# Optimization experiments

Measured on AMD Instinct MI355X. Metric: run time of the kernel, lower is better.

## Reference

```python
import jax, jax.numpy as jnp
import numpy as np

NUM_HEADS = 8
LN_EPS = 1e-5


def setup_inputs() -> dict:
    key = jax.random.key(0)
    ks = jax.random.split(key, 5)
    B, C, H, W = 4, 256, 48, 48
    scale = 1.0 / np.sqrt(C)
    return {
        "x": jax.random.normal(ks[0], (B, C, H, W), dtype=jnp.float32),
        "Wq": jax.random.normal(ks[1], (C, C), dtype=jnp.float32) * scale,
        "Wk": jax.random.normal(ks[2], (C, C), dtype=jnp.float32) * scale,
        "Wv": jax.random.normal(ks[3], (C, C), dtype=jnp.float32) * scale,
        "Wo": jax.random.normal(ks[4], (C, C), dtype=jnp.float32) * scale,
        "gamma": jnp.ones((C,), dtype=jnp.float32),
        "beta": jnp.zeros((C,), dtype=jnp.float32),
    }


def reference(x, Wq, Wk, Wv, Wo, gamma, beta):
    B, C, H, W = x.shape
    hd = C // NUM_HEADS
    N = H * W
    xf = x.reshape(B, C, N)  # [B, C, N]
    # 1x1 conv (no bias) == channel matmul, then split heads: [B, h, d, N]
    def proj(Wm):
        return jnp.einsum('oc,bcn->bon', Wm, xf).reshape(B, NUM_HEADS, hd, N)
    q = proj(Wq)
    k = proj(Wk)
    v = proj(Wv)
    # scores[b,h,i,j] = sum_d q[b,h,d,i] k[b,h,d,j] / sqrt(hd)
    scores = jnp.einsum('bhdi,bhdj->bhij', q, k) / jnp.sqrt(jnp.float32(hd))
    attn = jax.nn.softmax(scores, axis=-1)  # [B, h, N, N]
    # attended[b,h,d,i] = sum_j v[b,h,d,j] attn[b,h,i,j]
    attended = jnp.einsum('bhdj,bhij->bhdi', v, attn).reshape(B, C, H, W)
    out = jnp.einsum('oc,bchw->bohw', Wo, attended) + x
    # LayerNorm over channels (applied in NHWC layout in original)
    mu = out.mean(axis=1, keepdims=True)
    var = out.var(axis=1, keepdims=True)
    out = (out - mu) * jax.lax.rsqrt(var + LN_EPS)
    out = out * gamma[None, :, None, None] + beta[None, :, None, None]
    return out
```

## Files before the change

### kernel.cpp

```cpp
#include <hip/hip_runtime.h>

#define DEVI __device__ __forceinline__

typedef __bf16 bf16x8 __attribute__((ext_vector_type(8)));
typedef float f32x4 __attribute__((ext_vector_type(4)));

#define QSCALE 0.25503488f

#if __has_builtin(__builtin_amdgcn_exp2f)
#define EXP2(x) __builtin_amdgcn_exp2f(x)
#else
#define EXP2(x) __expf(0.69314718055994531f * (x))
#endif

DEVI unsigned short bfbits(float f) {
  union { __bf16 h; unsigned short u; } x;
  x.h = (__bf16)f;
  return x.u;
}
DEVI unsigned packbf2(float a, float b) {
  return (unsigned)bfbits(a) | ((unsigned)bfbits(b) << 16);
}
DEVI float bflo(unsigned u) { return __uint_as_float(u << 16); }
DEVI float bfhi(unsigned u) { return __uint_as_float(u & 0xffff0000u); }

DEVI void gload16(const unsigned short* g, void* l) {
  __builtin_amdgcn_global_load_lds((__attribute__((address_space(1))) const unsigned*)g,
                                   (__attribute__((address_space(3))) unsigned*)l, 16, 0, 0);
}

__global__ __launch_bounds__(256) void k_prep_x(const float* __restrict__ x,
                                                unsigned short* __restrict__ xT) {
  __shared__ float tile[64][65];
  const int b = blockIdx.x, n0 = blockIdx.y * 64, c0 = blockIdx.z * 64;
  const int t = threadIdx.x, tn = t & 63, tg = t >> 6;
  const float* xp = x + ((size_t)b * 256 + c0) * 2304 + n0;
#pragma unroll
  for (int i = 0; i < 16; ++i) {
    const int c = tg * 16 + i;
    tile[c][tn] = xp[(size_t)c * 2304 + tn];
  }
  __syncthreads();
  unsigned short* op = xT + ((size_t)b * 2304 + n0) * 256 + c0;
#pragma unroll
  for (int i = 0; i < 16; ++i) {
    const int n = tg * 16 + i;
    op[(size_t)n * 256 + tn] = bfbits(tile[tn][n]);
  }
}

__global__ __launch_bounds__(256) void k_prep_wo(const float* __restrict__ Wo,
                                                 unsigned short* __restrict__ WoB) {
  const int i = (blockIdx.x * 256 + threadIdx.x) * 4;
  const float4 v = *(const float4*)(Wo + i);
  uint2 u;
  u.x = packbf2(v.x, v.y);
  u.y = packbf2(v.z, v.w);
  *(uint2*)(WoB + i) = u;
}

__global__ __launch_bounds__(256) void k_proj_qk(const unsigned short* __restrict__ xT,
                                                 const float* __restrict__ Wq,
                                                 const float* __restrict__ Wk,
                                                 unsigned short* __restrict__ qhm,
                                                 unsigned short* __restrict__ khm) {
  __shared__ __align__(16) unsigned char wlds[32768];
  const int l = threadIdx.x & 63, w = threadIdx.x >> 6;
  const int lr = l & 15, lg = l >> 4;
  const int row0 = blockIdx.x * 64 + w * 16;
  const int h = blockIdx.y;
  {
    const int t = threadIdx.x;
    const int mat = t >> 7;
    const int t2 = t & 127;
    const int row = t2 >> 2;
    const int cj0 = (t2 & 3) * 8;
    const float* wp = (mat ? Wk : Wq) + (size_t)(h * 32 + row) * 256;
    unsigned char* ldst = wlds + mat * 16384 + row * 512;
#pragma unroll
    for (int i = 0; i < 8; ++i) {
      const int cj = cj0 + i;
      const float4 v0 = *(const float4*)(wp + cj * 8);
      const float4 v1 = *(const float4*)(wp + cj * 8 + 4);
      uint4 u;
      u.x = packbf2(v0.x, v0.y);
      u.y = packbf2(v0.z, v0.w);
      u.z = packbf2(v1.x, v1.y);
      u.w = packbf2(v1.z, v1.w);
      *(uint4*)(ldst + ((cj * 16) ^ ((row & 7) << 4))) = u;
    }
  }
  __syncthreads();

  f32x4 acc[2][2];
#pragma unroll
  for (int i = 0; i < 2; ++i)
#pragma unroll
    for (int j = 0; j < 2; ++j) acc[i][j] = (f32x4){0.f, 0.f, 0.f, 0.f};
  for (int ks = 0; ks < 8; ++ks) {
    const int c = ks * 32 + lg * 8;
    const bf16x8 a = *(const bf16x8*)(xT + (size_t)(row0 + lr) * 256 + c);
    bf16x8 bfr[2][2];
#pragma unroll
    for (int ot = 0; ot < 2; ++ot) {
      const int brow = ot * 16 + lr;
      const unsigned off = (unsigned)(brow * 512) + (((unsigned)((ks * 4 + lg) * 16)) ^ ((brow & 7) << 4));
      bfr[0][ot] = *(const bf16x8*)(wlds + off);
      bfr[1][ot] = *(const bf16x8*)(wlds + 16384 + off);
    }
#pragma unroll
    for (int m = 0; m < 2; ++m)
#pragma unroll
      for (int ot = 0; ot < 2; ++ot)
        acc[m][ot] = __builtin_amdgcn_mfma_f32_16x16x32_bf16(a, bfr[m][ot], acc[m][ot], 0, 0, 0);
  }
  const int b = row0 / 2304;
  const int nloc = row0 - b * 2304;
  const size_t slab = (size_t)(b * 8 + h) * 2304;
#pragma unroll
  for (int m = 0; m < 2; ++m) {
    unsigned short* outp = m ? khm : qhm;
    const float scale = m ? 1.0f : QSCALE;
#pragma unroll
    for (int ot = 0; ot < 2; ++ot)
#pragma unroll
      for (int r = 0; r < 4; ++r) {
        const int n = nloc + lg * 4 + r;
        const int d = ot * 16 + lr;
        outp[(slab + n) * 32 + d] = bfbits(acc[m][ot][r] * scale);
      }
  }
}

__global__ __launch_bounds__(256) void k_proj_v(const unsigned short* __restrict__ xT,
                                                const float* __restrict__ Wv,
                                                unsigned short* __restrict__ vN) {
  __shared__ __align__(16) unsigned char wlds[32768];
  const int l = threadIdx.x & 63, w = threadIdx.x >> 6;
  const int lr = l & 15, lg = l >> 4;
  const int rowbase = blockIdx.x * 64;
  const int col0 = blockIdx.y * 32;
  {
    const int t = threadIdx.x;
    const int row = t >> 2;
    const int cj0 = (t & 3) * 8;
    const float* wp = Wv + (size_t)(rowbase + row) * 256;
    unsigned char* ldst = wlds + row * 512;
#pragma unroll
    for (int i = 0; i < 8; ++i) {
      const int cj = cj0 + i;
      const float4 v0 = *(const float4*)(wp + cj * 8);
      const float4 v1 = *(const float4*)(wp + cj * 8 + 4);
      uint4 u;
      u.x = packbf2(v0.x, v0.y);
      u.y = packbf2(v0.z, v0.w);
      u.z = packbf2(v1.x, v1.y);
      u.w = packbf2(v1.z, v1.w);
      *(uint4*)(ldst + ((cj * 16) ^ ((row & 7) << 4))) = u;
    }
  }
  __syncthreads();

  f32x4 acc[2];
  acc[0] = (f32x4){0.f, 0.f, 0.f, 0.f};
  acc[1] = (f32x4){0.f, 0.f, 0.f, 0.f};
  for (int ks = 0; ks < 8; ++ks) {
    const int c = ks * 32 + lg * 8;
    bf16x8 a, bfr[2];
    const int arow = w * 16 + lr;
    a = *(const bf16x8*)(wlds + arow * 512 + (((unsigned)((ks * 4 + lg) * 16)) ^ ((arow & 7) << 4)));
#pragma unroll
    for (int nt = 0; nt < 2; ++nt)
      bfr[nt] = *(const bf16x8*)(xT + (size_t)(col0 + nt * 16 + lr) * 256 + c);
#pragma unroll
    for (int nt = 0; nt < 2; ++nt)
      acc[nt] = __builtin_amdgcn_mfma_f32_16x16x32_bf16(a, bfr[nt], acc[nt], 0, 0, 0);
  }
  const int b = blockIdx.y / 72, nb = (blockIdx.y % 72) * 32;
#pragma unroll
  for (int nt = 0; nt < 2; ++nt)
#pragma unroll
    for (int r = 0; r < 4; ++r) {
      const int o = rowbase + w * 16 + lg * 4 + r;
      const int n = nb + nt * 16 + lr;
      vN[(size_t)b * 589824 + (size_t)o * 2304 + n] = bfbits(acc[nt][r]);
    }
}

template <bool DIRECT>
__global__ __launch_bounds__(256) void k_attn(const unsigned short* __restrict__ qhm,
                                              const unsigned short* __restrict__ khm,
                                              const unsigned short* __restrict__ vN,
                                              unsigned short* __restrict__ partO,
                                              float* __restrict__ partS,
                                              unsigned short* __restrict__ attT,
                                              int tpc) {
  __shared__ __align__(16) unsigned char sm[32768];
  const int l = threadIdx.x & 63, w = threadIdx.x >> 6;
  const int lr = l & 15, lg = l >> 4;
  const int bh = blockIdx.y, b = bh >> 3, h = bh & 7;
  const int i0 = blockIdx.x * 128 + w * 32;
  const int c = blockIdx.z, t0 = c * tpc;
  unsigned char* smw = sm + w * 4096;
  const size_t slab = (size_t)bh * 2304;

  bf16x8 qf[2];
  {
    const unsigned short* qbase = qhm + (slab + i0) * 32;
#pragma unroll
    for (int it = 0; it < 2; ++it)
      qf[it] = *(const bf16x8*)(qbase + (it * 16 + lr) * 32 + lg * 8);
  }

  bf16x8 ones;
#pragma unroll
  for (int e = 0; e < 8; ++e) ones[e] = (__bf16)1.0f;

  f32x4 oacc[2][2];
#pragma unroll
  for (int i = 0; i < 2; ++i)
#pragma unroll
    for (int j = 0; j < 2; ++j) oacc[i][j] = (f32x4){0.f, 0.f, 0.f, 0.f};
  f32x4 psum[2];
  psum[0] = (f32x4){0.f, 0.f, 0.f, 0.f};
  psum[1] = (f32x4){0.f, 0.f, 0.f, 0.f};

  const unsigned short* kbase = khm + slab * 32 + (size_t)(64 * w + (l ^ ((l >> 2) & 3))) * 8;
  const int vks = w >> 1;
  const int vlg = (w * 2 + (l >> 5)) & 3;
  const unsigned short* vsrc = vN + (size_t)(b * 256 + h * 32 + (l & 31)) * 2304 + vks * 32 + vlg * 8;
  const int kdst = 16384 + w * 1024;
  const int vdst = 24576 + w * 1024;
  const int kxor = ((lg ^ (lr & 3)) << 4);

  gload16(kbase + (size_t)t0 * 2048, sm + kdst);
  gload16(vsrc + t0 * 64, sm + vdst);
  __syncthreads();

  for (int tt = 0; tt < tpc; ++tt) {
    const int buf = tt & 1;
    if (tt < tpc - 1) {
      const int nbuf = (tt + 1) & 1;
      gload16(kbase + (size_t)(t0 + tt + 1) * 2048, sm + kdst + nbuf * 4096);
      gload16(vsrc + (t0 + tt + 1) * 64, sm + vdst + nbuf * 4096);
    }

    const unsigned char* kb = sm + 16384 + buf * 4096;
    const unsigned char* vb = sm + 24576 + buf * 4096;

    bf16x8 kf[4];
    {
      const unsigned char* kread = kb + lr * 64 + kxor;
#pragma unroll
      for (int jt = 0; jt < 4; ++jt)
        kf[jt] = *(const bf16x8*)(kread + jt * 1024);
    }

    f32x4 s[4][2];
    const f32x4 zf = (f32x4){0.f, 0.f, 0.f, 0.f};
#pragma unroll
    for (int jt = 0; jt < 4; ++jt)
#pragma unroll
      for (int it = 0; it < 2; ++it)
        s[jt][it] = __builtin_amdgcn_mfma_f32_16x16x32_bf16(kf[jt], qf[it], zf, 0, 0, 0);

#pragma unroll
    for (int it = 0; it < 2; ++it) {
      const int iloc = it * 16 + lr;
      const unsigned swz = (unsigned)((iloc & 7) << 4);
      unsigned char* prow = smw + iloc * 128;
#pragma unroll
      for (int jt = 0; jt < 4; ++jt) {
        const float p0 = EXP2(s[jt][it][0]);
        const float p1 = EXP2(s[jt][it][1]);
        const float p2 = EXP2(s[jt][it][2]);
        const float p3 = EXP2(s[jt][it][3]);
        const unsigned jb = (unsigned)(jt * 32 + lg * 8);
        uint2 u;
        u.x = packbf2(p0, p1);
        u.y = packbf2(p2, p3);
        *(uint2*)(prow + (jb ^ swz)) = u;
      }
    }

    bf16x8 vf[2][2], pf[2][2];
#pragma unroll
    for (int dt = 0; dt < 2; ++dt)
#pragma unroll
      for (int ks = 0; ks < 2; ++ks)
        vf[dt][ks] = *(const bf16x8*)(vb + ks * 2048 + lg * 512 + (dt * 16 + lr) * 16);
#pragma unroll
    for (int it = 0; it < 2; ++it) {
      const int iloc = it * 16 + lr;
      const unsigned swz = (unsigned)((iloc & 7) << 4);
#pragma unroll
      for (int ks = 0; ks < 2; ++ks)
        pf[it][ks] = *(const bf16x8*)(smw + iloc * 128 + ((unsigned)(ks * 64 + lg * 16) ^ swz));
    }
#pragma unroll
    for (int dt = 0; dt < 2; ++dt)
#pragma unroll
      for (int it = 0; it < 2; ++it) {
        oacc[dt][it] = __builtin_amdgcn_mfma_f32_16x16x32_bf16(vf[dt][0], pf[it][0], oacc[dt][it], 0, 0, 0);
        oacc[dt][it] = __builtin_amdgcn_mfma_f32_16x16x32_bf16(vf[dt][1], pf[it][1], oacc[dt][it], 0, 0, 0);
      }
#pragma unroll
    for (int it = 0; it < 2; ++it) {
      psum[it] = __builtin_amdgcn_mfma_f32_16x16x32_bf16(ones, pf[it][0], psum[it], 0, 0, 0);
      psum[it] = __builtin_amdgcn_mfma_f32_16x16x32_bf16(ones, pf[it][1], psum[it], 0, 0, 0);
    }
    __syncthreads();
  }

  if (DIRECT) {
#pragma unroll
    for (int it = 0; it < 2; ++it) {
      const float inv = 1.0f / psum[it][0];
      const int iloc = it * 16 + lr;
      unsigned char* orow = smw + iloc * 68;
#pragma unroll
      for (int dt = 0; dt < 2; ++dt) {
        const int d = dt * 16 + lg * 4;
        *(unsigned*)(orow + d * 2) = packbf2(oacc[dt][it][0] * inv, oacc[dt][it][1] * inv);
        *(unsigned*)(orow + d * 2 + 4) = packbf2(oacc[dt][it][2] * inv, oacc[dt][it][3] * inv);
      }
    }
    __syncthreads();
    unsigned* attu = (unsigned*)attT;
#pragma unroll
    for (int it2 = 0; it2 < 8; ++it2) {
      const int lin = it2 * 64 + l;
      const int row = lin >> 4, k = lin & 15;
      const unsigned u = *(const unsigned*)(smw + row * 68 + k * 4);
      attu[(size_t)(b * 2304 + i0 + row) * 128 + h * 16 + k] = u;
    }
  } else {
    const size_t pbase = ((size_t)(c * 32 + bh) * 2304 + i0) * 32;
#pragma unroll
    for (int it = 0; it < 2; ++it)
#pragma unroll
      for (int dt = 0; dt < 2; ++dt) {
        const size_t addr = pbase + (size_t)(it * 16 + lr) * 32 + dt * 16 + lg * 4;
        uint2 u;
        u.x = packbf2(oacc[dt][it][0], oacc[dt][it][1]);
        u.y = packbf2(oacc[dt][it][2], oacc[dt][it][3]);
        *(uint2*)(partO + addr) = u;
      }
    if (lg == 0) {
      const size_t sbase = (size_t)(c * 32 + bh) * 2304 + i0;
      partS[sbase + lr] = psum[0][0];
      partS[sbase + 16 + lr] = psum[1][0];
    }
  }
}

template <bool COMBINE>
__global__ __launch_bounds__(256) void k_out_ln(const unsigned short* __restrict__ Wo,
                                                const unsigned short* __restrict__ attT,
                                                const unsigned short* __restrict__ partO,
                                                const float* __restrict__ partS,
                                                int nc,
                                                const float* __restrict__ x,
                                                const float* __restrict__ gamma,
                                                const float* __restrict__ beta,
                                                float* __restrict__ out) {
  __shared__ __align__(16) unsigned char alds[8192];
  __shared__ float wsum[4][16], wsq[4][16], smean[16], srstd[16];
  const int l = threadIdx.x & 63, w = threadIdx.x >> 6;
  const int lr = l & 15, lg = l >> 4;
  const int b = blockIdx.x / 144;
  const int n0 = (blockIdx.x % 144) * 16;
  const int row0 = w * 64;
  const size_t bn0 = (size_t)b * 2304 + n0;

  if (COMBINE) {
    const int t = threadIdx.x;
    const int row = t >> 4;
    const int i = n0 + row;
    const int cj0 = (t & 15) * 2;
#pragma unroll
    for (int ii = 0; ii < 2; ++ii) {
      const int cj = cj0 + ii;
      const int h = cj >> 2;
      const int d0 = (cj & 3) * 8;
      const int bh8 = b * 8 + h;
      float ssum = 0.f;
      float a0 = 0.f, a1 = 0.f, a2 = 0.f, a3 = 0.f, a4 = 0.f, a5 = 0.f, a6 = 0.f, a7 = 0.f;
      for (int cz = 0; cz < nc; ++cz) {
        const size_t rbase = (size_t)(cz * 32 + bh8) * 2304 + i;
        ssum += partS[rbase];
        const uint4 v = *(const uint4*)(partO + rbase * 32 + d0);
        a0 += bflo(v.x); a1 += bfhi(v.x);
        a2 += bflo(v.y); a3 += bfhi(v.y);
        a4 += bflo(v.z); a5 += bfhi(v.z);
        a6 += bflo(v.w); a7 += bfhi(v.w);
      }
      const float inv = 1.0f / ssum;
      uint4 u;
      u.x = packbf2(a0 * inv, a1 * inv);
      u.y = packbf2(a2 * inv, a3 * inv);
      u.z = packbf2(a4 * inv, a5 * inv);
      u.w = packbf2(a6 * inv, a7 * inv);
      *(uint4*)(alds + row * 512 + ((cj * 16) ^ ((row & 7) << 4))) = u;
    }
  } else {
    const int t = threadIdx.x;
    const int row = t >> 4;
    const int cj0 = (t & 15) * 2;
#pragma unroll
    for (int ii = 0; ii < 2; ++ii) {
      const int cj = cj0 + ii;
      const uint4 v = *(const uint4*)(attT + (bn0 + row) * 256 + cj * 8);
      *(uint4*)(alds + row * 512 + ((cj * 16) ^ ((row & 7) << 4))) = v;
    }
  }
  __syncthreads();

  f32x4 acc[4];
#pragma unroll
  for (int i = 0; i < 4; ++i) acc[i] = (f32x4){0.f, 0.f, 0.f, 0.f};
  for (int ks = 0; ks < 8; ++ks) {
    const int c = ks * 32 + lg * 8;
    bf16x8 a[4], bb;
#pragma unroll
    for (int rt = 0; rt < 4; ++rt)
      a[rt] = *(const bf16x8*)(Wo + (size_t)(row0 + rt * 16 + lr) * 256 + c);
    bb = *(const bf16x8*)(alds + lr * 512 + (((unsigned)((ks * 4 + lg) * 16)) ^ ((lr & 7) << 4)));
#pragma unroll
    for (int rt = 0; rt < 4; ++rt)
      acc[rt] = __builtin_amdgcn_mfma_f32_16x16x32_bf16(a[rt], bb, acc[rt], 0, 0, 0);
  }
  const float* xb = x + (size_t)b * 589824;
  float vals[4][4];
  float s0 = 0.f, q0 = 0.f;
#pragma unroll
  for (int rt = 0; rt < 4; ++rt)
#pragma unroll
    for (int r = 0; r < 4; ++r) {
      const int o = row0 + rt * 16 + lg * 4 + r;
      const int n = n0 + lr;
      const float vv = acc[rt][r] + xb[(size_t)o * 2304 + n];
      vals[rt][r] = vv;
      s0 += vv;
      q0 += vv * vv;
    }
  s0 += __shfl_xor(s0, 16); s0 += __shfl_xor(s0, 32);
  q0 += __shfl_xor(q0, 16); q0 += __shfl_xor(q0, 32);
  if (l < 16) {
    wsum[w][l] = s0;
    wsq[w][l] = q0;
  }
  __syncthreads();
  if (threadIdx.x < 16) {
    const int c16 = threadIdx.x;
    const float S = wsum[0][c16] + wsum[1][c16] + wsum[2][c16] + wsum[3][c16];
    const float Q = wsq[0][c16] + wsq[1][c16] + wsq[2][c16] + wsq[3][c16];
    const float mean = S * (1.0f / 256.0f);
    const float var = Q * (1.0f / 256.0f) - mean * mean;
    smean[c16] = mean;
    srstd[c16] = rsqrtf(var + 1e-5f);
  }
  __syncthreads();
  {
    const float mean = smean[lr];
    const float rstd = srstd[lr];
    const int n = n0 + lr;
#pragma unroll
    for (int rt = 0; rt < 4; ++rt)
#pragma unroll
      for (int r = 0; r < 4; ++r) {
        const int o = row0 + rt * 16 + lg * 4 + r;
        out[(size_t)b * 589824 + (size_t)o * 2304 + n] =
            (vals[rt][r] - mean) * rstd * gamma[o] + beta[o];
      }
  }
}

extern "C" void kernel_launch(void* const* d_in, const int* in_sizes, int n_in,
                              void* d_out, int out_size, void* d_ws, size_t ws_size,
                              hipStream_t stream) {
  (void)in_sizes; (void)n_in; (void)out_size;
  const float* x = (const float*)d_in[0];
  const float* Wq = (const float*)d_in[1];
  const float* Wk = (const float*)d_in[2];
  const float* Wv = (const float*)d_in[3];
  const float* Wo = (const float*)d_in[4];
  const float* gamma = (const float*)d_in[5];
  const float* beta = (const float*)d_in[6];
  float* out = (float*)d_out;
  char* ws = (char*)d_ws;
  unsigned short* attT = (unsigned short*)(ws);
  unsigned short* qhm = (unsigned short*)(ws + 4718592);
  unsigned short* khm = (unsigned short*)(ws + 9437184);
  unsigned short* vN = (unsigned short*)(ws + 14155776);
  unsigned short* xT = (unsigned short*)(ws + 18874368);
  unsigned short* WoB = qhm;

  const size_t base = 18874368;
  const size_t chunk = 4718592 + 294912;
  const size_t need4 = base + 4 * chunk;
  const size_t need2 = base + 2 * chunk;
  const int nc = (ws_size >= need4) ? 4 : (ws_size >= need2) ? 2 : 1;
  unsigned short* partO = (unsigned short*)(ws + base);
  float* partS = (float*)(ws + base + (size_t)nc * 4718592);

  k_prep_x<<<dim3(4, 36, 4), 256, 0, stream>>>(x, xT);
  k_proj_qk<<<dim3(144, 8), 256, 0, stream>>>(xT, Wq, Wk, qhm, khm);
  k_proj_v<<<dim3(4, 288), 256, 0, stream>>>(xT, Wv, vN);
  if (nc > 1) {
    k_attn<false><<<dim3(18, 32, nc), 256, 0, stream>>>(qhm, khm, vN, partO, partS, attT, 36 / nc);
    k_prep_wo<<<dim3(64), 256, 0, stream>>>(Wo, WoB);
    k_out_ln<true><<<dim3(576), 256, 0, stream>>>(WoB, attT, partO, partS, nc, x, gamma, beta, out);
  } else {
    k_attn<true><<<dim3(18, 32, 1), 256, 0, stream>>>(qhm, khm, vN, attT, (float*)attT, attT, 36);
    k_prep_wo<<<dim3(64), 256, 0, stream>>>(Wo, WoB);
    k_out_ln<false><<<dim3(576), 256, 0, stream>>>(WoB, attT, partO, partS, 1, x, gamma, beta, out);
  }
}
```

Baseline: 171.3 us.

## Fuse x transpose, QKV projections and Wo conversion into one kernel

Replaces the separate x-transpose, Q/K projection, V projection and Wo-conversion kernels with a single kernel. Each of the 144 blocks transposes a 64-position tile of x into a bf16 LDS tile and computes Q, K and V for all heads from it, so the xT workspace round trip and three launches go away. 16 extra blocks convert Wo. The cost is a grid of only 160 blocks of 256 threads with about 96KB of LDS each, which lowers parallelism and occupancy, and each block now serialises loops over all weight chunks.

```diff
diff --git a/kernel.cpp b/kernel.cpp
--- a/kernel.cpp
+++ b/kernel.cpp
@@ -29,162 +29,167 @@
                                    (__attribute__((address_space(3))) unsigned*)l, 16, 0, 0);
 }
 
-__global__ __launch_bounds__(256) void k_prep_x(const float* __restrict__ x,
-                                                unsigned short* __restrict__ xT) {
-  __shared__ float tile[64][65];
-  const int b = blockIdx.x, n0 = blockIdx.y * 64, c0 = blockIdx.z * 64;
-  const int t = threadIdx.x, tn = t & 63, tg = t >> 6;
-  const float* xp = x + ((size_t)b * 256 + c0) * 2304 + n0;
-#pragma unroll
-  for (int i = 0; i < 16; ++i) {
-    const int c = tg * 16 + i;
-    tile[c][tn] = xp[(size_t)c * 2304 + tn];
-  }
-  __syncthreads();
-  unsigned short* op = xT + ((size_t)b * 2304 + n0) * 256 + c0;
-#pragma unroll
-  for (int i = 0; i < 16; ++i) {
-    const int n = tg * 16 + i;
-    op[(size_t)n * 256 + tn] = bfbits(tile[tn][n]);
-  }
-}
-
-__global__ __launch_bounds__(256) void k_prep_wo(const float* __restrict__ Wo,
-                                                 unsigned short* __restrict__ WoB) {
-  const int i = (blockIdx.x * 256 + threadIdx.x) * 4;
-  const float4 v = *(const float4*)(Wo + i);
-  uint2 u;
-  u.x = packbf2(v.x, v.y);
-  u.y = packbf2(v.z, v.w);
-  *(uint2*)(WoB + i) = u;
-}
-
-__global__ __launch_bounds__(256) void k_proj_qk(const unsigned short* __restrict__ xT,
-                                                 const float* __restrict__ Wq,
-                                                 const float* __restrict__ Wk,
-                                                 unsigned short* __restrict__ qhm,
-                                                 unsigned short* __restrict__ khm) {
-  __shared__ __align__(16) unsigned char wlds[32768];
-  const int l = threadIdx.x & 63, w = threadIdx.x >> 6;
+__global__ __launch_bounds__(256) void k_qkv(const float* __restrict__ x,
+                                             const float* __restrict__ Wq,
+                                             const float* __restrict__ Wk,
+                                             const float* __restrict__ Wv,
+                                             const float* __restrict__ Wo,
+                                             unsigned short* __restrict__ qhm,
+                                             unsigned short* __restrict__ khm,
+                                             unsigned short* __restrict__ vN,
+                                             unsigned short* __restrict__ WoB) {
+  const int bid = blockIdx.x;
+  const int t = threadIdx.x;
+  if (bid >= 144) {
+    const int i = ((bid - 144) * 256 + t) * 16;
+#pragma unroll
+    for (int j = 0; j < 4; ++j) {
+      const float4 v = *(const float4*)(Wo + i + j * 4);
+      uint2 u;
+      u.x = packbf2(v.x, v.y);
+      u.y = packbf2(v.z, v.w);
+      *(uint2*)(WoB + i + j * 4) = u;
+    }
+    return;
+  }
+  __shared__ __align__(16) unsigned char xtile[32768];
+  __shared__ __align__(16) unsigned char wtile[32768];
+  __shared__ __align__(16) unsigned char wtile2[32768];
+  const int b = bid / 36, n0 = (bid % 36) * 64;
+  const int l = t & 63, w = t >> 6;
   const int lr = l & 15, lg = l >> 4;
-  const int row0 = blockIdx.x * 64 + w * 16;
-  const int h = blockIdx.y;
-  {
-    const int t = threadIdx.x;
-    const int mat = t >> 7;
-    const int t2 = t & 127;
-    const int row = t2 >> 2;
-    const int cj0 = (t2 & 3) * 8;
-    const float* wp = (mat ? Wk : Wq) + (size_t)(h * 32 + row) * 256;
-    unsigned char* ldst = wlds + mat * 16384 + row * 512;
-#pragma unroll
-    for (int i = 0; i < 8; ++i) {
-      const int cj = cj0 + i;
-      const float4 v0 = *(const float4*)(wp + cj * 8);
-      const float4 v1 = *(const float4*)(wp + cj * 8 + 4);
-      uint4 u;
-      u.x = packbf2(v0.x, v0.y);
-      u.y = packbf2(v0.z, v0.w);
-      u.z = packbf2(v1.x, v1.y);
-      u.w = packbf2(v1.z, v1.w);
-      *(uint4*)(ldst + ((cj * 16) ^ ((row & 7) << 4))) = u;
-    }
-  }
-  __syncthreads();
-
-  f32x4 acc[2][2];
-#pragma unroll
-  for (int i = 0; i < 2; ++i)
-#pragma unroll
-    for (int j = 0; j < 2; ++j) acc[i][j] = (f32x4){0.f, 0.f, 0.f, 0.f};
-  for (int ks = 0; ks < 8; ++ks) {
-    const int c = ks * 32 + lg * 8;
-    const bf16x8 a = *(const bf16x8*)(xT + (size_t)(row0 + lr) * 256 + c);
-    bf16x8 bfr[2][2];
-#pragma unroll
-    for (int ot = 0; ot < 2; ++ot) {
-      const int brow = ot * 16 + lr;
-      const unsigned off = (unsigned)(brow * 512) + (((unsigned)((ks * 4 + lg) * 16)) ^ ((brow & 7) << 4));
-      bfr[0][ot] = *(const bf16x8*)(wlds + off);
-      bfr[1][ot] = *(const bf16x8*)(wlds + 16384 + off);
-    }
-#pragma unroll
-    for (int m = 0; m < 2; ++m)
-#pragma unroll
-      for (int ot = 0; ot < 2; ++ot)
-        acc[m][ot] = __builtin_amdgcn_mfma_f32_16x16x32_bf16(a, bfr[m][ot], acc[m][ot], 0, 0, 0);
-  }
-  const int b = row0 / 2304;
-  const int nloc = row0 - b * 2304;
-  const size_t slab = (size_t)(b * 8 + h) * 2304;
-#pragma unroll
-  for (int m = 0; m < 2; ++m) {
-    unsigned short* outp = m ? khm : qhm;
-    const float scale = m ? 1.0f : QSCALE;
-#pragma unroll
-    for (int ot = 0; ot < 2; ++ot)
+  const int tn = t & 63, tg = t >> 6;
+
+  float* tmp = (float*)wtile;
+  for (int cb = 0; cb < 4; ++cb) {
+    const float* xp = x + ((size_t)b * 256 + cb * 64) * 2304 + n0;
+#pragma unroll
+    for (int i = 0; i < 16; ++i) {
+      const int c = tg * 16 + i;
+      tmp[c * 65 + tn] = xp[(size_t)c * 2304 + tn];
+    }
+    __syncthreads();
+    {
+      unsigned u[8];
+#pragma unroll
+      for (int j = 0; j < 8; ++j)
+        u[j] = packbf2(tmp[(tg * 16 + 2 * j) * 65 + tn], tmp[(tg * 16 + 2 * j + 1) * 65 + tn]);
+      unsigned char* dst = xtile + tn * 512;
+      const unsigned base = (unsigned)(cb * 128 + tg * 32);
+      const unsigned swz = (unsigned)((tn & 7) << 4);
+      *(uint4*)(dst + (base ^ swz)) = *(uint4*)&u[0];
+      *(uint4*)(dst + ((base + 16) ^ swz)) = *(uint4*)&u[4];
+    }
+    __syncthreads();
+  }
+
+  bf16x8 a[8];
+#pragma unroll
+  for (int ks = 0; ks < 8; ++ks)
+    a[ks] = *(const bf16x8*)(xtile + (w * 16 + lr) * 512 +
+                             (((unsigned)((ks * 4 + lg) * 16)) ^ ((lr & 7) << 4)));
+
+  for (int oc = 0; oc < 4; ++oc) {
+    {
+      const int mat = t >> 7;
+      const int t2 = t & 127;
+      const int row = t2 >> 1;
+      const int cj0 = (t2 & 1) * 16;
+      const float* wp = (mat ? Wk : Wq) + (size_t)(oc * 64 + row) * 256;
+      unsigned char* ldst = (mat ? wtile2 : wtile) + row * 512;
+      const unsigned swz = (unsigned)((row & 7) << 4);
+#pragma unroll
+      for (int i = 0; i < 16; ++i) {
+        const int cj = cj0 + i;
+        const float4 v0 = *(const float4*)(wp + cj * 8);
+        const float4 v1 = *(const float4*)(wp + cj * 8 + 4);
+        uint4 u;
+        u.x = packbf2(v0.x, v0.y);
+        u.y = packbf2(v0.z, v0.w);
+        u.z = packbf2(v1.x, v1.y);
+        u.w = packbf2(v1.z, v1.w);
+        *(uint4*)(ldst + (((unsigned)(cj * 16)) ^ swz)) = u;
+      }
+    }
+    __syncthreads();
+#pragma unroll
+    for (int m = 0; m < 2; ++m) {
+      const unsigned char* wsrc = m ? wtile2 : wtile;
+      unsigned short* outp = m ? khm : qhm;
+      const float scale = m ? 1.0f : QSCALE;
+      f32x4 acc[4];
+#pragma unroll
+      for (int ot = 0; ot < 4; ++ot) acc[ot] = (f32x4){0.f, 0.f, 0.f, 0.f};
+      for (int ks = 0; ks < 8; ++ks) {
+#pragma unroll
+        for (int ot = 0; ot < 4; ++ot) {
+          const int brow = ot * 16 + lr;
+          const bf16x8 bfr = *(const bf16x8*)(wsrc + brow * 512 +
+                                              (((unsigned)((ks * 4 + lg) * 16)) ^ ((brow & 7) << 4)));
+          acc[ot] = __builtin_amdgcn_mfma_f32_16x16x32_bf16(a[ks], bfr, acc[ot], 0, 0, 0);
+        }
+      }
+#pragma unroll
+      for (int ot = 0; ot < 4; ++ot) {
+        const int h = 2 * oc + (ot >> 1);
+        const int d = (ot & 1) * 16 + lr;
+        const size_t slab = (size_t)(b * 8 + h) * 2304;
+#pragma unroll
+        for (int r = 0; r < 4; ++r) {
+          const int n = n0 + w * 16 + lg * 4 + r;
+          outp[(slab + n) * 32 + d] = bfbits(acc[ot][r] * scale);
+        }
+      }
+    }
+    __syncthreads();
+  }
+
+  for (int oc = 0; oc < 4; ++oc) {
+    {
+      const int row = t >> 2;
+      const int cj0 = (t & 3) * 8;
+      const float* wp = Wv + (size_t)(oc * 64 + row) * 256;
+      unsigned char* ldst = wtile + row * 512;
+      const unsigned swz = (unsigned)((row & 7) << 4);
+#pragma unroll
+      for (int i = 0; i < 8; ++i) {
+        const int cj = cj0 + i;
+        const float4 v0 = *(const float4*)(wp + cj * 8);
+        const float4 v1 = *(const float4*)(wp + cj * 8 + 4);
+        uint4 u;
+        u.x = packbf2(v0.x, v0.y);
+        u.y = packbf2(v0.z, v0.w);
+        u.z = packbf2(v1.x, v1.y);
+        u.w = packbf2(v1.z, v1.w);
+        *(uint4*)(ldst + (((unsigned)(cj * 16)) ^ swz)) = u;
+      }
+    }
+    __syncthreads();
+    f32x4 acc[4];
+#pragma unroll
+    for (int nt = 0; nt < 4; ++nt) acc[nt] = (f32x4){0.f, 0.f, 0.f, 0.f};
+    for (int ks = 0; ks < 8; ++ks) {
+      const int arow = w * 16 + lr;
+      const bf16x8 aw = *(const bf16x8*)(wtile + arow * 512 +
+                                         (((unsigned)((ks * 4 + lg) * 16)) ^ ((arow & 7) << 4)));
+#pragma unroll
+      for (int nt = 0; nt < 4; ++nt) {
+        const int brow = nt * 16 + lr;
+        const bf16x8 bx = *(const bf16x8*)(xtile + brow * 512 +
+                                           (((unsigned)((ks * 4 + lg) * 16)) ^ ((brow & 7) << 4)));
+        acc[nt] = __builtin_amdgcn_mfma_f32_16x16x32_bf16(aw, bx, acc[nt], 0, 0, 0);
+      }
+    }
+#pragma unroll
+    for (int nt = 0; nt < 4; ++nt)
 #pragma unroll
       for (int r = 0; r < 4; ++r) {
-        const int n = nloc + lg * 4 + r;
-        const int d = ot * 16 + lr;
-        outp[(slab + n) * 32 + d] = bfbits(acc[m][ot][r] * scale);
-      }
-  }
-}
-
-__global__ __launch_bounds__(256) void k_proj_v(const unsigned short* __restrict__ xT,
-                                                const float* __restrict__ Wv,
-                                                unsigned short* __restrict__ vN) {
-  __shared__ __align__(16) unsigned char wlds[32768];
-  const int l = threadIdx.x & 63, w = threadIdx.x >> 6;
-  const int lr = l & 15, lg = l >> 4;
-  const int rowbase = blockIdx.x * 64;
-  const int col0 = blockIdx.y * 32;
-  {
-    const int t = threadIdx.x;
-    const int row = t >> 2;
-    const int cj0 = (t & 3) * 8;
-    const float* wp = Wv + (size_t)(rowbase + row) * 256;
-    unsigned char* ldst = wlds + row * 512;
-#pragma unroll
-    for (int i = 0; i < 8; ++i) {
-      const int cj = cj0 + i;
-      const float4 v0 = *(const float4*)(wp + cj * 8);
-      const float4 v1 = *(const float4*)(wp + cj * 8 + 4);
-      uint4 u;
-      u.x = packbf2(v0.x, v0.y);
-      u.y = packbf2(v0.z, v0.w);
-      u.z = packbf2(v1.x, v1.y);
-      u.w = packbf2(v1.z, v1.w);
-      *(uint4*)(ldst + ((cj * 16) ^ ((row & 7) << 4))) = u;
-    }
-  }
-  __syncthreads();
-
-  f32x4 acc[2];
-  acc[0] = (f32x4){0.f, 0.f, 0.f, 0.f};
-  acc[1] = (f32x4){0.f, 0.f, 0.f, 0.f};
-  for (int ks = 0; ks < 8; ++ks) {
-    const int c = ks * 32 + lg * 8;
-    bf16x8 a, bfr[2];
-    const int arow = w * 16 + lr;
-    a = *(const bf16x8*)(wlds + arow * 512 + (((unsigned)((ks * 4 + lg) * 16)) ^ ((arow & 7) << 4)));
-#pragma unroll
-    for (int nt = 0; nt < 2; ++nt)
-      bfr[nt] = *(const bf16x8*)(xT + (size_t)(col0 + nt * 16 + lr) * 256 + c);
-#pragma unroll
-    for (int nt = 0; nt < 2; ++nt)
-      acc[nt] = __builtin_amdgcn_mfma_f32_16x16x32_bf16(a, bfr[nt], acc[nt], 0, 0, 0);
-  }
-  const int b = blockIdx.y / 72, nb = (blockIdx.y % 72) * 32;
-#pragma unroll
-  for (int nt = 0; nt < 2; ++nt)
-#pragma unroll
-    for (int r = 0; r < 4; ++r) {
-      const int o = rowbase + w * 16 + lg * 4 + r;
-      const int n = nb + nt * 16 + lr;
-      vN[(size_t)b * 589824 + (size_t)o * 2304 + n] = bfbits(acc[nt][r]);
-    }
+        const int o = oc * 64 + w * 16 + lg * 4 + r;
+        const int n = n0 + nt * 16 + lr;
+        vN[(size_t)b * 589824 + (size_t)o * 2304 + n] = bfbits(acc[nt][r]);
+      }
+    __syncthreads();
+  }
 }
 
 template <bool DIRECT>
@@ -489,31 +494,25 @@
   const float* beta = (const float*)d_in[6];
   float* out = (float*)d_out;
   char* ws = (char*)d_ws;
-  unsigned short* attT = (unsigned short*)(ws);
-  unsigned short* qhm = (unsigned short*)(ws + 4718592);
-  unsigned short* khm = (unsigned short*)(ws + 9437184);
-  unsigned short* vN = (unsigned short*)(ws + 14155776);
-  unsigned short* xT = (unsigned short*)(ws + 18874368);
-  unsigned short* WoB = qhm;
-
-  const size_t base = 18874368;
+  unsigned short* qhm = (unsigned short*)(ws);
+  unsigned short* khm = (unsigned short*)(ws + 4718592);
+  unsigned short* vN = (unsigned short*)(ws + 9437184);
+  unsigned short* WoB = (unsigned short*)(ws + 14155776);
+  const size_t pbase = 14286848;
   const size_t chunk = 4718592 + 294912;
-  const size_t need4 = base + 4 * chunk;
-  const size_t need2 = base + 2 * chunk;
+  const size_t need4 = pbase + 4 * chunk;
+  const size_t need2 = pbase + 2 * chunk;
   const int nc = (ws_size >= need4) ? 4 : (ws_size >= need2) ? 2 : 1;
-  unsigned short* partO = (unsigned short*)(ws + base);
-  float* partS = (float*)(ws + base + (size_t)nc * 4718592);
-
-  k_prep_x<<<dim3(4, 36, 4), 256, 0, stream>>>(x, xT);
-  k_proj_qk<<<dim3(144, 8), 256, 0, stream>>>(xT, Wq, Wk, qhm, khm);
-  k_proj_v<<<dim3(4, 288), 256, 0, stream>>>(xT, Wv, vN);
+  unsigned short* partO = (unsigned short*)(ws + pbase);
+  float* partS = (float*)(ws + pbase + (size_t)nc * 4718592);
+  unsigned short* attT = (unsigned short*)(ws + pbase);
+
+  k_qkv<<<dim3(160), 256, 0, stream>>>(x, Wq, Wk, Wv, Wo, qhm, khm, vN, WoB);
   if (nc > 1) {
     k_attn<false><<<dim3(18, 32, nc), 256, 0, stream>>>(qhm, khm, vN, partO, partS, attT, 36 / nc);
-    k_prep_wo<<<dim3(64), 256, 0, stream>>>(Wo, WoB);
     k_out_ln<true><<<dim3(576), 256, 0, stream>>>(WoB, attT, partO, partS, nc, x, gamma, beta, out);
   } else {
     k_attn<true><<<dim3(18, 32, 1), 256, 0, stream>>>(qhm, khm, vN, attT, (float*)attT, attT, 36);
-    k_prep_wo<<<dim3(64), 256, 0, stream>>>(Wo, WoB);
     k_out_ln<false><<<dim3(576), 256, 0, stream>>>(WoB, attT, partO, partS, 1, x, gamma, beta, out);
   }
 }
```

Result: no change. 172.2 us (+0.6%).
